# Optimization experiments

Measured on AMD Instinct MI355X. Metric: run time of the kernel, lower is better.

The kernel has to match this reference:

```python
import jax, jax.numpy as jnp
import numpy as np

B, S, D, H = 4, 2048, 512, 8
HD = D // H  # head_size = 64


def setup_inputs() -> dict:
    key = jax.random.key(0)
    ks = jax.random.split(key, 11)
    sd = 1.0 / np.sqrt(D)
    return {
        "q": jax.random.normal(ks[0], (B, S, D), jnp.float32),
        "k": jax.random.normal(ks[1], (B, S, D), jnp.float32),
        "v": jax.random.normal(ks[2], (B, S, D), jnp.float32),
        "Wq": jax.random.normal(ks[3], (D, D), jnp.float32) * sd,
        "bq": jnp.zeros((D,), jnp.float32),
        "Wk": jax.random.normal(ks[4], (D, D), jnp.float32) * sd,
        "bk": jnp.zeros((D,), jnp.float32),
        "Wv": jax.random.normal(ks[5], (D, D), jnp.float32) * sd,
        "bv": jnp.zeros((D,), jnp.float32),
        "Wo": jax.random.normal(ks[6], (D, D), jnp.float32) * sd,
        "bo": jnp.zeros((D,), jnp.float32),
    }


def _split_heads(x):
    # [B,S,D] -> [B,H,S,HD]
    return x.reshape(B, S, H, HD).transpose(0, 2, 1, 3)


def reference(q, k, v, Wq, bq, Wk, bk, Wv, bv, Wo, bo):
    qp = _split_heads(q @ Wq.T + bq)
    kp = _split_heads(k @ Wk.T + bk)
    vp = _split_heads(v @ Wv.T + bv)
    scale = 1.0 / jnp.sqrt(jnp.float32(HD))
    scores = jnp.einsum("bhqd,bhkd->bhqk", qp, kp) * scale  # [B,H,S,S]
    weights = jax.nn.softmax(scores, axis=-1)
    ctx = jnp.einsum("bhqk,bhkd->bhqd", weights, vp)
    ctx = ctx.transpose(0, 2, 1, 3).reshape(B, S, D)
    return ctx @ Wo.T + bo
```

## Files before the change

kernel.cpp:

```cpp
#include <hip/hip_runtime.h>
#include <hip/hip_bf16.h>
#include <stdint.h>

#define BB   4
#define SS   2048
#define DDIM 512
#define HH   8
#define HDIM 64
#define MTOT (BB*SS)
#define QSCALE (0.125f * 1.44269504088896340736f)

typedef __bf16 bf16;
typedef __bf16 bf16x8 __attribute__((ext_vector_type(8)));
typedef float  f32x4  __attribute__((ext_vector_type(4)));

__device__ __forceinline__ f32x4 mfma32(bf16x8 a, bf16x8 b, f32x4 c) {
    return __builtin_amdgcn_mfma_f32_16x16x32_bf16(a, b, c, 0, 0, 0);
}

__device__ __forceinline__ void gload_lds16(const void* g, void* l) {
    __builtin_amdgcn_global_load_lds(
        (__attribute__((address_space(1))) unsigned int*)(uintptr_t)g,
        (__attribute__((address_space(3))) unsigned int*)l,
        16, 0, 0);
}

__device__ __forceinline__ short bf16bits(float f) {
    union { __bf16 h; short s; } u; u.h = (__bf16)f; return u.s;
}

__global__ void cvt_kernel(const float* __restrict__ q, const float* __restrict__ k,
                           const float* __restrict__ v, const float* __restrict__ w0,
                           const float* __restrict__ w1, const float* __restrict__ w2,
                           const float* __restrict__ w3,
                           bf16* __restrict__ dq, bf16* __restrict__ dk,
                           bf16* __restrict__ dv, bf16* __restrict__ dw0,
                           bf16* __restrict__ dw1, bf16* __restrict__ dw2,
                           bf16* __restrict__ dw3) {
    const float* s; bf16* d; int n4;
    switch (blockIdx.y) {
        case 0: s = q;  d = dq;  n4 = (BB*SS*DDIM)/4; break;
        case 1: s = k;  d = dk;  n4 = (BB*SS*DDIM)/4; break;
        case 2: s = v;  d = dv;  n4 = (BB*SS*DDIM)/4; break;
        case 3: s = w0; d = dw0; n4 = (DDIM*DDIM)/4; break;
        case 4: s = w1; d = dw1; n4 = (DDIM*DDIM)/4; break;
        case 5: s = w2; d = dw2; n4 = (DDIM*DDIM)/4; break;
        default: s = w3; d = dw3; n4 = (DDIM*DDIM)/4; break;
    }
    int stride = gridDim.x * blockDim.x;
    for (int i = blockIdx.x * blockDim.x + threadIdx.x; i < n4; i += stride) {
        float4 f = ((const float4*)s)[i];
        union { bf16 h[4]; uint2 u; } o;
        o.h[0] = (bf16)f.x; o.h[1] = (bf16)f.y; o.h[2] = (bf16)f.z; o.h[3] = (bf16)f.w;
        ((uint2*)d)[i] = o.u;
    }
}

#define GEMM_BODY(A_, W_, K_, MB_, NB_)                                          \
    __shared__ bf16 As[2][128 * 64];                                             \
    __shared__ bf16 Bs[2][128 * 64];                                             \
    const int tid = threadIdx.x;                                                 \
    const int w = tid >> 6, lane = tid & 63;                                     \
    const int c15 = lane & 15, quad = lane >> 4;                                 \
    const int mblk = (MB_), nblk = (NB_);                                        \
    const int wm = (w & 1) * 64, wn = (w >> 1) * 64;                             \
    f32x4 acc[4][4] = {};                                                        \
    const bf16* Ablk = (A_) + (size_t)mblk * (K_);                               \
    const bf16* Bblk = (W_) + (size_t)nblk * (K_);                               \
    int g_off[4], l_base[4];                                                     \
    _Pragma("unroll")                                                            \
    for (int ci = 0; ci < 4; ++ci) {                                             \
        const int s = (w * 4 + ci) * 64 + lane;                                  \
        const int kr = s >> 3, kc = (s & 7) ^ (kr & 7);                          \
        g_off[ci] = kr * (K_) + kc * 8;                                          \
        l_base[ci] = (w * 4 + ci) * 512;                                         \
    }                                                                            \
    _Pragma("unroll")                                                            \
    for (int ci = 0; ci < 4; ++ci) {                                             \
        gload_lds16(Ablk + g_off[ci], &As[0][l_base[ci]]);                       \
        gload_lds16(Bblk + g_off[ci], &Bs[0][l_base[ci]]);                       \
    }                                                                            \
    int bufi = 0;                                                                \
    for (int kt = 0; kt < (K_); kt += 64) {                                      \
        __syncthreads();              \
        if (kt + 64 < (K_)) {                                                    \
            _Pragma("unroll")                                                    \
            for (int ci = 0; ci < 4; ++ci) {                                     \
                gload_lds16(Ablk + g_off[ci] + kt + 64, &As[bufi ^ 1][l_base[ci]]); \
                gload_lds16(Bblk + g_off[ci] + kt + 64, &Bs[bufi ^ 1][l_base[ci]]); \
            }                                                                    \
        }                                                                        \
        _Pragma("unroll")                                                        \
        for (int hh = 0; hh < 2; ++hh) {                                         \
            bf16x8 af[4], bfr[4];                                                \
            _Pragma("unroll")                                                    \
            for (int i = 0; i < 4; ++i) {                                        \
                const int row = wm + i * 16 + c15;                               \
                af[i] = *(const bf16x8*)&As[bufi][row * 64 + (((hh * 4 + quad) ^ (row & 7)) * 8)]; \
            }                                                                    \
            _Pragma("unroll")                                                    \
            for (int j = 0; j < 4; ++j) {                                        \
                const int row = wn + j * 16 + c15;                               \
                bfr[j] = *(const bf16x8*)&Bs[bufi][row * 64 + (((hh * 4 + quad) ^ (row & 7)) * 8)]; \
            }                                                                    \
            _Pragma("unroll")                                                    \
            for (int i = 0; i < 4; ++i)                                          \
                _Pragma("unroll")                                                \
                for (int j = 0; j < 4; ++j)                                      \
                    acc[i][j] = mfma32(af[i], bfr[j], acc[i][j]);                \
        }                                                                        \
        bufi ^= 1;                                                               \
    }

__global__ __launch_bounds__(256)
void proj_gemm(const bf16* __restrict__ Aq, const bf16* __restrict__ Ak,
               const bf16* __restrict__ Av,
               const bf16* __restrict__ Wq, const bf16* __restrict__ Wk,
               const bf16* __restrict__ Wv,
               const float* __restrict__ bq, const float* __restrict__ bk,
               const float* __restrict__ bv,
               bf16* __restrict__ Qp, bf16* __restrict__ Kp, bf16* __restrict__ Vt2) {
    const int mode = blockIdx.z;
    const bf16* A;  const bf16* Wm; const float* bias;
    int mb, nb;
    if (mode == 0)      { A = Aq; Wm = Wq; bias = bq; mb = blockIdx.x * 128; nb = blockIdx.y * 128; }
    else if (mode == 1) { A = Ak; Wm = Wk; bias = bk; mb = blockIdx.x * 128; nb = blockIdx.y * 128; }
    else {
        const int id = blockIdx.y * 64 + blockIdx.x;
        A = Wv; Wm = Av; bias = bv; mb = (id & 3) * 128; nb = (id >> 2) * 128;
    }
    GEMM_BODY(A, Wm, DDIM, mb, nb)
    if (mode == 2) {
        #pragma unroll
        for (int i = 0; i < 4; ++i) {
            #pragma unroll
            for (int r = 0; r < 4; ++r) {
                const int row = mblk + wm + i * 16 + quad * 4 + r;
                const float bval = bias[row];
                #pragma unroll
                for (int j = 0; j < 4; ++j) {
                    const int col = nblk + wn + j * 16 + c15;
                    const int colp = (col & ~31) + (c15 >> 2) * 8 + (j & 1) * 4 + (c15 & 3);
                    Vt2[(size_t)row * MTOT + colp] = (bf16)(acc[i][j][r] + bval);
                }
            }
        }
    } else {
        #pragma unroll
        for (int j = 0; j < 4; ++j) {
            const int col = nblk + wn + j * 16 + c15;
            const int h = col >> 6, hd = col & 63;
            const float bval = bias[col];
            #pragma unroll
            for (int i = 0; i < 4; ++i) {
                #pragma unroll
                for (int r = 0; r < 4; ++r) {
                    const int row = mblk + wm + i * 16 + quad * 4 + r;
                    const int b = row >> 11, s = row & (SS - 1);
                    float v = acc[i][j][r] + bval;
                    if (mode == 0) v *= QSCALE;
                    bf16* dst = (mode == 0) ? Qp : Kp;
                    dst[(((size_t)(b * HH + h)) * SS + s) * HDIM + hd] = (bf16)v;
                }
            }
        }
    }
}

__global__ __launch_bounds__(256)
void out_gemm(const bf16* __restrict__ A, const bf16* __restrict__ Wo,
              const float* __restrict__ bo, float* __restrict__ Out) {
    GEMM_BODY(A, Wo, DDIM, blockIdx.x * 128, blockIdx.y * 128)
    #pragma unroll
    for (int j = 0; j < 4; ++j) {
        const int col = nblk + wn + j * 16 + c15;
        const float bval = bo[col];
        #pragma unroll
        for (int i = 0; i < 4; ++i) {
            #pragma unroll
            for (int r = 0; r < 4; ++r) {
                const int row = mblk + wm + i * 16 + quad * 4 + r;
                Out[(size_t)row * DDIM + col] = acc[i][j][r] + bval;
            }
        }
    }
}

__global__ __launch_bounds__(256, 2)
void attn_kernel(const bf16* __restrict__ Qp, const bf16* __restrict__ Kp,
                 const bf16* __restrict__ Vt2, bf16* __restrict__ Ctx) {
    __shared__ bf16 Klds[2][128 * 64];
    __shared__ bf16 Vlds[2][64 * 128];

    const int tid = threadIdx.x;
    const int w = tid >> 6, lane = tid & 63;
    const int c15 = lane & 15, quad = lane >> 4;
    const int bh = blockIdx.y;
    const int b = bh >> 3, h = bh & 7;
    const int qbase = blockIdx.x * 128;

    const bf16* Qh = Qp + (size_t)bh * SS * HDIM;
    const bf16* Kh = Kp + (size_t)bh * SS * HDIM;
    const bf16* Vh = Vt2 + (size_t)h * HDIM * MTOT + (size_t)b * SS;

    bf16x8 qf[2][2];
    #pragma unroll
    for (int g = 0; g < 2; ++g) {
        const int qrow = qbase + w * 32 + g * 16 + c15;
        qf[g][0] = *(const bf16x8*)&Qh[(size_t)qrow * HDIM + quad * 8];
        qf[g][1] = *(const bf16x8*)&Qh[(size_t)qrow * HDIM + 32 + quad * 8];
    }

    int koff[4], voff[4];
    #pragma unroll
    for (int ci = 0; ci < 4; ++ci) {
        const int s = (w * 4 + ci) * 64 + lane;
        const int kr = s >> 3, kc = (s & 7) ^ (kr & 7);
        koff[ci] = kr * HDIM + kc * 8;
        const int vr = s >> 4, vc = (s & 15) ^ (vr & 15);
        voff[ci] = vr * MTOT + vc * 8;
    }

    union FragS { short s[8]; bf16x8 v; };
    FragS idf, ones8;
    #pragma unroll
    for (int j = 0; j < 8; ++j) {
        idf.s[j] = (j < 4 && quad * 4 + j == c15) ? (short)0x3F80 : (short)0;
        ones8.s[j] = (short)0x3F80;
    }

    f32x4 oacc[2][4] = {};
    f32x4 lacc[2] = {};
    const int ksw = c15 & 7;

    #pragma unroll
    for (int ci = 0; ci < 4; ++ci) {
        gload_lds16(Kh + koff[ci], &Klds[0][(w * 4 + ci) * 512]);
        gload_lds16(Vh + voff[ci], &Vlds[0][(w * 4 + ci) * 512]);
    }

    int buf = 0;
    for (int kt = 0; kt < SS; kt += 128) {
        __syncthreads();
        if (kt + 128 < SS) {
            const bf16* Ks = Kh + (size_t)(kt + 128) * HDIM;
            const bf16* Vs = Vh + (kt + 128);
            #pragma unroll
            for (int ci = 0; ci < 4; ++ci) {
                gload_lds16(Ks + koff[ci], &Klds[buf ^ 1][(w * 4 + ci) * 512]);
                gload_lds16(Vs + voff[ci], &Vlds[buf ^ 1][(w * 4 + ci) * 512]);
            }
        }

        FragS paf[2][4];
        #pragma unroll
        for (int nt = 0; nt < 8; ++nt) {
            const int krow = nt * 16 + c15;
            bf16x8 kb0 = *(const bf16x8*)&Klds[buf][(krow * 8 + (quad ^ ksw)) * 8];
            bf16x8 kb1 = *(const bf16x8*)&Klds[buf][(krow * 8 + ((quad + 4) ^ ksw)) * 8];
            #pragma unroll
            for (int g = 0; g < 2; ++g) {
                f32x4 z = {};
                z = mfma32(qf[g][0], kb0, z);
                z = mfma32(qf[g][1], kb1, z);
                FragS pk;
                #pragma unroll
                for (int r = 0; r < 4; ++r)
                    pk.s[r] = bf16bits(__builtin_amdgcn_exp2f(z[r]));
                pk.s[4] = pk.s[5] = pk.s[6] = pk.s[7] = 0;
                f32x4 zero = {};
                f32x4 t = mfma32(pk.v, idf.v, zero);
                const int half = (nt & 1) * 4;
                #pragma unroll
                for (int r = 0; r < 4; ++r)
                    paf[g][nt >> 1].s[half + r] = bf16bits(t[r]);
            }
        }

        #pragma unroll
        for (int t = 0; t < 4; ++t) {
            lacc[0] = mfma32(paf[0][t].v, ones8.v, lacc[0]);
            lacc[1] = mfma32(paf[1][t].v, ones8.v, lacc[1]);
            #pragma unroll
            for (int j = 0; j < 4; ++j) {
                const int row = j * 16 + c15;
                bf16x8 vb = *(const bf16x8*)&Vlds[buf][row * 128 +
                            (((4 * t + quad) ^ c15) * 8)];
                oacc[0][j] = mfma32(paf[0][t].v, vb, oacc[0][j]);
                oacc[1][j] = mfma32(paf[1][t].v, vb, oacc[1][j]);
            }
        }
        buf ^= 1;
    }

    bf16* Cb = Ctx + ((size_t)b * SS) * DDIM + (size_t)h * HDIM;
    #pragma unroll
    for (int g = 0; g < 2; ++g)
        #pragma unroll
        for (int r = 0; r < 4; ++r) {
            const int row = qbase + w * 32 + g * 16 + quad * 4 + r;
            const float inv = 1.0f / lacc[g][r];
            #pragma unroll
            for (int j = 0; j < 4; ++j) {
                const int hd = j * 16 + c15;
                Cb[(size_t)row * DDIM + hd] = (bf16)(oacc[g][j][r] * inv);
            }
        }
}

extern "C" void kernel_launch(void* const* d_in, const int* in_sizes, int n_in,
                              void* d_out, int out_size, void* d_ws, size_t ws_size,
                              hipStream_t stream) {
    const float* q  = (const float*)d_in[0];
    const float* k  = (const float*)d_in[1];
    const float* v  = (const float*)d_in[2];
    const float* Wq = (const float*)d_in[3];
    const float* bq = (const float*)d_in[4];
    const float* Wk = (const float*)d_in[5];
    const float* bk = (const float*)d_in[6];
    const float* Wv = (const float*)d_in[7];
    const float* bv = (const float*)d_in[8];
    const float* Wo = (const float*)d_in[9];
    const float* bo = (const float*)d_in[10];
    float* out = (float*)d_out;

    const size_t SZ_T = (size_t)BB * SS * DDIM * 2;
    const size_t SZ_W = (size_t)DDIM * DDIM * 2;
    char* ws = (char*)d_ws;
    bf16* qb  = (bf16*)(ws + 0 * SZ_T);
    bf16* kb  = (bf16*)(ws + 1 * SZ_T);
    bf16* vb  = (bf16*)(ws + 2 * SZ_T);
    bf16* Wqb = (bf16*)(ws + 3 * SZ_T + 0 * SZ_W);
    bf16* Wkb = (bf16*)(ws + 3 * SZ_T + 1 * SZ_W);
    bf16* Wvb = (bf16*)(ws + 3 * SZ_T + 2 * SZ_W);
    bf16* Wob = (bf16*)(ws + 3 * SZ_T + 3 * SZ_W);
    bf16* Qp  = (bf16*)(ws + 3 * SZ_T + 4 * SZ_W);
    bf16* Kp  = (bf16*)(ws + 4 * SZ_T + 4 * SZ_W);
    bf16* Vt2 = (bf16*)(ws + 5 * SZ_T + 4 * SZ_W);
    bf16* ctx = (bf16*)(ws + 6 * SZ_T + 4 * SZ_W);
    const size_t needed = 7 * SZ_T + 4 * SZ_W;
    if (ws_size < needed) return;

    cvt_kernel<<<dim3(512, 7), 256, 0, stream>>>(q, k, v, Wq, Wk, Wv, Wo,
                                                 qb, kb, vb, Wqb, Wkb, Wvb, Wob);
    proj_gemm<<<dim3(MTOT / 128, DDIM / 128, 3), 256, 0, stream>>>(
        qb, kb, vb, Wqb, Wkb, Wvb, bq, bk, bv, Qp, Kp, Vt2);
    attn_kernel<<<dim3(SS / 128, BB * HH), 256, 0, stream>>>(Qp, Kp, Vt2, ctx);
    out_gemm<<<dim3(MTOT / 128, DDIM / 128), 256, 0, stream>>>(ctx, Wob, bo, out);
}
```

Before: 191.6 us.

## Fuse fp32-to-bf16 conversion into GEMM loads and drop identity-MFMA transpose in attention

Removes the separate conversion kernel. The projection and output GEMMs now load fp32 inputs into registers, convert them to bf16, and write them to LDS inside the double-buffered loop. In attention, the QK MFMA operands are swapped so the score fragment comes out already in the layout the PV MFMA needs, which removes the exp/identity-MFMA transpose step. This cuts a full bf16 round trip of q, k and v through HBM and some MFMA work, at the cost of register-staged loads instead of direct-to-LDS loads in the projection GEMM.

```diff
diff --git a/kernel.cpp b/kernel.cpp
--- a/kernel.cpp
+++ b/kernel.cpp
@@ -29,34 +29,14 @@
     union { __bf16 h; short s; } u; u.h = (__bf16)f; return u.s;
 }
 
-__global__ void cvt_kernel(const float* __restrict__ q, const float* __restrict__ k,
-                           const float* __restrict__ v, const float* __restrict__ w0,
-                           const float* __restrict__ w1, const float* __restrict__ w2,
-                           const float* __restrict__ w3,
-                           bf16* __restrict__ dq, bf16* __restrict__ dk,
-                           bf16* __restrict__ dv, bf16* __restrict__ dw0,
-                           bf16* __restrict__ dw1, bf16* __restrict__ dw2,
-                           bf16* __restrict__ dw3) {
-    const float* s; bf16* d; int n4;
-    switch (blockIdx.y) {
-        case 0: s = q;  d = dq;  n4 = (BB*SS*DDIM)/4; break;
-        case 1: s = k;  d = dk;  n4 = (BB*SS*DDIM)/4; break;
-        case 2: s = v;  d = dv;  n4 = (BB*SS*DDIM)/4; break;
-        case 3: s = w0; d = dw0; n4 = (DDIM*DDIM)/4; break;
-        case 4: s = w1; d = dw1; n4 = (DDIM*DDIM)/4; break;
-        case 5: s = w2; d = dw2; n4 = (DDIM*DDIM)/4; break;
-        default: s = w3; d = dw3; n4 = (DDIM*DDIM)/4; break;
-    }
-    int stride = gridDim.x * blockDim.x;
-    for (int i = blockIdx.x * blockDim.x + threadIdx.x; i < n4; i += stride) {
-        float4 f = ((const float4*)s)[i];
-        union { bf16 h[4]; uint2 u; } o;
-        o.h[0] = (bf16)f.x; o.h[1] = (bf16)f.y; o.h[2] = (bf16)f.z; o.h[3] = (bf16)f.w;
-        ((uint2*)d)[i] = o.u;
-    }
-}
-
-#define GEMM_BODY(A_, W_, K_, MB_, NB_)                                          \
+__device__ __forceinline__ void cvt_write8(float4 a, float4 b, bf16* dst) {
+    union { bf16 h[8]; uint4 u; } o;
+    o.h[0] = (bf16)a.x; o.h[1] = (bf16)a.y; o.h[2] = (bf16)a.z; o.h[3] = (bf16)a.w;
+    o.h[4] = (bf16)b.x; o.h[5] = (bf16)b.y; o.h[6] = (bf16)b.z; o.h[7] = (bf16)b.w;
+    *(uint4*)dst = o.u;
+}
+
+#define GEMM_CORE(A_, AF32_, W_, WF32_, K_, MB_, NB_)                            \
     __shared__ bf16 As[2][128 * 64];                                             \
     __shared__ bf16 Bs[2][128 * 64];                                             \
     const int tid = threadIdx.x;                                                 \
@@ -65,29 +45,50 @@
     const int mblk = (MB_), nblk = (NB_);                                        \
     const int wm = (w & 1) * 64, wn = (w >> 1) * 64;                             \
     f32x4 acc[4][4] = {};                                                        \
-    const bf16* Ablk = (A_) + (size_t)mblk * (K_);                               \
-    const bf16* Bblk = (W_) + (size_t)nblk * (K_);                               \
-    int g_off[4], l_base[4];                                                     \
+    int soff[4], goff[4];                                                        \
     _Pragma("unroll")                                                            \
     for (int ci = 0; ci < 4; ++ci) {                                             \
         const int s = (w * 4 + ci) * 64 + lane;                                  \
         const int kr = s >> 3, kc = (s & 7) ^ (kr & 7);                          \
-        g_off[ci] = kr * (K_) + kc * 8;                                          \
-        l_base[ci] = (w * 4 + ci) * 512;                                         \
+        soff[ci] = s * 8;                                                        \
+        goff[ci] = kr * (K_) + kc * 8;                                           \
+    }                                                                            \
+    const float* ap32 = (const float*)(A_) + (size_t)mblk * (K_);                \
+    const float* bp32 = (const float*)(W_) + (size_t)nblk * (K_);                \
+    const bf16*  ap16 = (const bf16*)(A_) + (size_t)mblk * (K_);                 \
+    const bf16*  bp16 = (const bf16*)(W_) + (size_t)nblk * (K_);                 \
+    float4 areg[4][2], breg[4][2];                                               \
+    _Pragma("unroll")                                                            \
+    for (int ci = 0; ci < 4; ++ci) {                                             \
+        if (AF32_) {                                                             \
+            areg[ci][0] = *(const float4*)(ap32 + goff[ci]);                     \
+            areg[ci][1] = *(const float4*)(ap32 + goff[ci] + 4);                 \
+        } else gload_lds16(ap16 + goff[ci], &As[0][soff[ci]]);                   \
+        if (WF32_) {                                                             \
+            breg[ci][0] = *(const float4*)(bp32 + goff[ci]);                     \
+            breg[ci][1] = *(const float4*)(bp32 + goff[ci] + 4);                 \
+        } else gload_lds16(bp16 + goff[ci], &Bs[0][soff[ci]]);                   \
     }                                                                            \
     _Pragma("unroll")                                                            \
     for (int ci = 0; ci < 4; ++ci) {                                             \
-        gload_lds16(Ablk + g_off[ci], &As[0][l_base[ci]]);                       \
-        gload_lds16(Bblk + g_off[ci], &Bs[0][l_base[ci]]);                       \
+        if (AF32_) cvt_write8(areg[ci][0], areg[ci][1], &As[0][soff[ci]]);       \
+        if (WF32_) cvt_write8(breg[ci][0], breg[ci][1], &Bs[0][soff[ci]]);       \
     }                                                                            \
     int bufi = 0;                                                                \
     for (int kt = 0; kt < (K_); kt += 64) {                                      \
-        __syncthreads();              \
-        if (kt + 64 < (K_)) {                                                    \
+        __syncthreads();                                                         \
+        const bool more = (kt + 64 < (K_));                                      \
+        if (more) {                                                              \
             _Pragma("unroll")                                                    \
             for (int ci = 0; ci < 4; ++ci) {                                     \
-                gload_lds16(Ablk + g_off[ci] + kt + 64, &As[bufi ^ 1][l_base[ci]]); \
-                gload_lds16(Bblk + g_off[ci] + kt + 64, &Bs[bufi ^ 1][l_base[ci]]); \
+                if (AF32_) {                                                     \
+                    areg[ci][0] = *(const float4*)(ap32 + goff[ci] + kt + 64);   \
+                    areg[ci][1] = *(const float4*)(ap32 + goff[ci] + kt + 68);   \
+                } else gload_lds16(ap16 + goff[ci] + kt + 64, &As[bufi ^ 1][soff[ci]]); \
+                if (WF32_) {                                                     \
+                    breg[ci][0] = *(const float4*)(bp32 + goff[ci] + kt + 64);   \
+                    breg[ci][1] = *(const float4*)(bp32 + goff[ci] + kt + 68);   \
+                } else gload_lds16(bp16 + goff[ci] + kt + 64, &Bs[bufi ^ 1][soff[ci]]); \
             }                                                                    \
         }                                                                        \
         _Pragma("unroll")                                                        \
@@ -109,27 +110,34 @@
                 for (int j = 0; j < 4; ++j)                                      \
                     acc[i][j] = mfma32(af[i], bfr[j], acc[i][j]);                \
         }                                                                        \
+        if (more) {                                                              \
+            _Pragma("unroll")                                                    \
+            for (int ci = 0; ci < 4; ++ci) {                                     \
+                if (AF32_) cvt_write8(areg[ci][0], areg[ci][1], &As[bufi ^ 1][soff[ci]]); \
+                if (WF32_) cvt_write8(breg[ci][0], breg[ci][1], &Bs[bufi ^ 1][soff[ci]]); \
+            }                                                                    \
+        }                                                                        \
         bufi ^= 1;                                                               \
     }
 
 __global__ __launch_bounds__(256)
-void proj_gemm(const bf16* __restrict__ Aq, const bf16* __restrict__ Ak,
-               const bf16* __restrict__ Av,
-               const bf16* __restrict__ Wq, const bf16* __restrict__ Wk,
-               const bf16* __restrict__ Wv,
+void proj_gemm(const float* __restrict__ q, const float* __restrict__ k,
+               const float* __restrict__ v,
+               const float* __restrict__ Wq, const float* __restrict__ Wk,
+               const float* __restrict__ Wv,
                const float* __restrict__ bq, const float* __restrict__ bk,
                const float* __restrict__ bv,
                bf16* __restrict__ Qp, bf16* __restrict__ Kp, bf16* __restrict__ Vt2) {
     const int mode = blockIdx.z;
-    const bf16* A;  const bf16* Wm; const float* bias;
+    const float* A; const float* Wm; const float* bias;
     int mb, nb;
-    if (mode == 0)      { A = Aq; Wm = Wq; bias = bq; mb = blockIdx.x * 128; nb = blockIdx.y * 128; }
-    else if (mode == 1) { A = Ak; Wm = Wk; bias = bk; mb = blockIdx.x * 128; nb = blockIdx.y * 128; }
+    if (mode == 0)      { A = q; Wm = Wq; bias = bq; mb = blockIdx.x * 128; nb = blockIdx.y * 128; }
+    else if (mode == 1) { A = k; Wm = Wk; bias = bk; mb = blockIdx.x * 128; nb = blockIdx.y * 128; }
     else {
         const int id = blockIdx.y * 64 + blockIdx.x;
-        A = Wv; Wm = Av; bias = bv; mb = (id & 3) * 128; nb = (id >> 2) * 128;
-    }
-    GEMM_BODY(A, Wm, DDIM, mb, nb)
+        A = Wv; Wm = v; bias = bv; mb = (id & 3) * 128; nb = (id >> 2) * 128;
+    }
+    GEMM_CORE(A, 1, Wm, 1, DDIM, mb, nb)
     if (mode == 2) {
         #pragma unroll
         for (int i = 0; i < 4; ++i) {
@@ -157,10 +165,10 @@
                 for (int r = 0; r < 4; ++r) {
                     const int row = mblk + wm + i * 16 + quad * 4 + r;
                     const int b = row >> 11, s = row & (SS - 1);
-                    float v = acc[i][j][r] + bval;
-                    if (mode == 0) v *= QSCALE;
+                    float vv = acc[i][j][r] + bval;
+                    if (mode == 0) vv *= QSCALE;
                     bf16* dst = (mode == 0) ? Qp : Kp;
-                    dst[(((size_t)(b * HH + h)) * SS + s) * HDIM + hd] = (bf16)v;
+                    dst[(((size_t)(b * HH + h)) * SS + s) * HDIM + hd] = (bf16)vv;
                 }
             }
         }
@@ -168,9 +176,9 @@
 }
 
 __global__ __launch_bounds__(256)
-void out_gemm(const bf16* __restrict__ A, const bf16* __restrict__ Wo,
+void out_gemm(const bf16* __restrict__ A, const float* __restrict__ Wo,
               const float* __restrict__ bo, float* __restrict__ Out) {
-    GEMM_BODY(A, Wo, DDIM, blockIdx.x * 128, blockIdx.y * 128)
+    GEMM_CORE(A, 0, Wo, 1, DDIM, blockIdx.x * 128, blockIdx.y * 128)
     #pragma unroll
     for (int j = 0; j < 4; ++j) {
         const int col = nblk + wn + j * 16 + c15;
@@ -222,12 +230,9 @@
     }
 
     union FragS { short s[8]; bf16x8 v; };
-    FragS idf, ones8;
-    #pragma unroll
-    for (int j = 0; j < 8; ++j) {
-        idf.s[j] = (j < 4 && quad * 4 + j == c15) ? (short)0x3F80 : (short)0;
-        ones8.s[j] = (short)0x3F80;
-    }
+    FragS ones8;
+    #pragma unroll
+    for (int j = 0; j < 8; ++j) ones8.s[j] = (short)0x3F80;
 
     f32x4 oacc[2][4] = {};
     f32x4 lacc[2] = {};
@@ -261,19 +266,13 @@
             #pragma unroll
             for (int g = 0; g < 2; ++g) {
                 f32x4 z = {};
-                z = mfma32(qf[g][0], kb0, z);
-                z = mfma32(qf[g][1], kb1, z);
-                FragS pk;
-                #pragma unroll
-                for (int r = 0; r < 4; ++r)
-                    pk.s[r] = bf16bits(__builtin_amdgcn_exp2f(z[r]));
-                pk.s[4] = pk.s[5] = pk.s[6] = pk.s[7] = 0;
-                f32x4 zero = {};
-                f32x4 t = mfma32(pk.v, idf.v, zero);
+                z = mfma32(kb0, qf[g][0], z);
+                z = mfma32(kb1, qf[g][1], z);
                 const int half = (nt & 1) * 4;
                 #pragma unroll
                 for (int r = 0; r < 4; ++r)
-                    paf[g][nt >> 1].s[half + r] = bf16bits(t[r]);
+                    paf[g][nt >> 1].s[half + r] =
+                        bf16bits(__builtin_amdgcn_exp2f(z[r]));
             }
         }
 
@@ -325,26 +324,16 @@
     float* out = (float*)d_out;
 
     const size_t SZ_T = (size_t)BB * SS * DDIM * 2;
-    const size_t SZ_W = (size_t)DDIM * DDIM * 2;
     char* ws = (char*)d_ws;
-    bf16* qb  = (bf16*)(ws + 0 * SZ_T);
-    bf16* kb  = (bf16*)(ws + 1 * SZ_T);
-    bf16* vb  = (bf16*)(ws + 2 * SZ_T);
-    bf16* Wqb = (bf16*)(ws + 3 * SZ_T + 0 * SZ_W);
-    bf16* Wkb = (bf16*)(ws + 3 * SZ_T + 1 * SZ_W);
-    bf16* Wvb = (bf16*)(ws + 3 * SZ_T + 2 * SZ_W);
-    bf16* Wob = (bf16*)(ws + 3 * SZ_T + 3 * SZ_W);
-    bf16* Qp  = (bf16*)(ws + 3 * SZ_T + 4 * SZ_W);
-    bf16* Kp  = (bf16*)(ws + 4 * SZ_T + 4 * SZ_W);
-    bf16* Vt2 = (bf16*)(ws + 5 * SZ_T + 4 * SZ_W);
-    bf16* ctx = (bf16*)(ws + 6 * SZ_T + 4 * SZ_W);
-    const size_t needed = 7 * SZ_T + 4 * SZ_W;
+    bf16* Qp  = (bf16*)(ws + 0 * SZ_T);
+    bf16* Kp  = (bf16*)(ws + 1 * SZ_T);
+    bf16* Vt2 = (bf16*)(ws + 2 * SZ_T);
+    bf16* ctx = (bf16*)(ws + 3 * SZ_T);
+    const size_t needed = 4 * SZ_T;
     if (ws_size < needed) return;
 
-    cvt_kernel<<<dim3(512, 7), 256, 0, stream>>>(q, k, v, Wq, Wk, Wv, Wo,
-                                                 qb, kb, vb, Wqb, Wkb, Wvb, Wob);
     proj_gemm<<<dim3(MTOT / 128, DDIM / 128, 3), 256, 0, stream>>>(
-        qb, kb, vb, Wqb, Wkb, Wvb, bq, bk, bv, Qp, Kp, Vt2);
+        q, k, v, Wq, Wk, Wv, bq, bk, bv, Qp, Kp, Vt2);
     attn_kernel<<<dim3(SS / 128, BB * HH), 256, 0, stream>>>(Qp, Kp, Vt2, ctx);
-    out_gemm<<<dim3(MTOT / 128, DDIM / 128), 256, 0, stream>>>(ctx, Wob, bo, out);
-}
+    out_gemm<<<dim3(MTOT / 128, DDIM / 128), 256, 0, stream>>>(ctx, Wo, bo, out);
+}
```

Result: no change. 190.3 us (-0.7%).

## Swap QK MFMA operands to drop identity transpose; halve GEMM K-tile

Applied to the files above, without the earlier changes.

In the attention loop, the QK^T MFMA now takes K as the A operand and Q as the B operand. The exp2 results therefore land directly in the layout the PV MFMA needs as its A fragment. This removes the per-tile identity-matrix MFMA and its extra bf16 conversions, which existed only to transpose the probabilities. Separately, the projection and output GEMMs shrink their K tile from 64 to 32 with a matching LDS swizzle and set launch bounds for 4 blocks per SU. That cuts LDS per block so more blocks can be resident, at the cost of twice as many barriers per GEMM.

```diff
diff --git a/kernel.cpp b/kernel.cpp
--- a/kernel.cpp
+++ b/kernel.cpp
@@ -56,80 +56,78 @@
     }
 }
 
-#define GEMM_BODY(A_, W_, K_, MB_, NB_)                                          \
-    __shared__ bf16 As[2][128 * 64];                                             \
-    __shared__ bf16 Bs[2][128 * 64];                                             \
+#define GEMM_CORE(A_, W_, K_, MB_, NB_)                                          \
+    __shared__ bf16 As[2][128 * 32];                                             \
+    __shared__ bf16 Bs[2][128 * 32];                                             \
     const int tid = threadIdx.x;                                                 \
     const int w = tid >> 6, lane = tid & 63;                                     \
     const int c15 = lane & 15, quad = lane >> 4;                                 \
     const int mblk = (MB_), nblk = (NB_);                                        \
     const int wm = (w & 1) * 64, wn = (w >> 1) * 64;                             \
     f32x4 acc[4][4] = {};                                                        \
-    const bf16* Ablk = (A_) + (size_t)mblk * (K_);                               \
-    const bf16* Bblk = (W_) + (size_t)nblk * (K_);                               \
-    int g_off[4], l_base[4];                                                     \
+    const bf16* Ab = (A_) + (size_t)mblk * (K_);                                 \
+    const bf16* Bb = (W_) + (size_t)nblk * (K_);                                 \
+    int goff[2], soff[2];                                                        \
     _Pragma("unroll")                                                            \
-    for (int ci = 0; ci < 4; ++ci) {                                             \
-        const int s = (w * 4 + ci) * 64 + lane;                                  \
-        const int kr = s >> 3, kc = (s & 7) ^ (kr & 7);                          \
-        g_off[ci] = kr * (K_) + kc * 8;                                          \
-        l_base[ci] = (w * 4 + ci) * 512;                                         \
+    for (int ci = 0; ci < 2; ++ci) {                                             \
+        const int s = (w * 2 + ci) * 64 + lane;                 \
+        const int kr = s >> 2;                                                   \
+        const int c = (s & 3) ^ ((kr >> 1) & 3);                                 \
+        goff[ci] = kr * (K_) + c * 8;                                            \
+        soff[ci] = s * 8;                                                        \
     }                                                                            \
     _Pragma("unroll")                                                            \
-    for (int ci = 0; ci < 4; ++ci) {                                             \
-        gload_lds16(Ablk + g_off[ci], &As[0][l_base[ci]]);                       \
-        gload_lds16(Bblk + g_off[ci], &Bs[0][l_base[ci]]);                       \
+    for (int ci = 0; ci < 2; ++ci) {                                             \
+        gload_lds16(Ab + goff[ci], &As[0][soff[ci]]);                            \
+        gload_lds16(Bb + goff[ci], &Bs[0][soff[ci]]);                            \
     }                                                                            \
     int bufi = 0;                                                                \
-    for (int kt = 0; kt < (K_); kt += 64) {                                      \
+    for (int kt = 0; kt < (K_); kt += 32) {                                      \
         __syncthreads();              \
-        if (kt + 64 < (K_)) {                                                    \
+        if (kt + 32 < (K_)) {                                                    \
             _Pragma("unroll")                                                    \
-            for (int ci = 0; ci < 4; ++ci) {                                     \
-                gload_lds16(Ablk + g_off[ci] + kt + 64, &As[bufi ^ 1][l_base[ci]]); \
-                gload_lds16(Bblk + g_off[ci] + kt + 64, &Bs[bufi ^ 1][l_base[ci]]); \
+            for (int ci = 0; ci < 2; ++ci) {                                     \
+                gload_lds16(Ab + goff[ci] + kt + 32, &As[bufi ^ 1][soff[ci]]);   \
+                gload_lds16(Bb + goff[ci] + kt + 32, &Bs[bufi ^ 1][soff[ci]]);   \
             }                                                                    \
         }                                                                        \
+        bf16x8 af[4], bfr[4];                                                    \
         _Pragma("unroll")                                                        \
-        for (int hh = 0; hh < 2; ++hh) {                                         \
-            bf16x8 af[4], bfr[4];                                                \
+        for (int i = 0; i < 4; ++i) {                                            \
+            const int row = wm + i * 16 + c15;                                   \
+            af[i] = *(const bf16x8*)&As[bufi][row * 32 + ((quad ^ ((row >> 1) & 3)) * 8)]; \
+        }                                                                        \
+        _Pragma("unroll")                                                        \
+        for (int j = 0; j < 4; ++j) {                                            \
+            const int row = wn + j * 16 + c15;                                   \
+            bfr[j] = *(const bf16x8*)&Bs[bufi][row * 32 + ((quad ^ ((row >> 1) & 3)) * 8)]; \
+        }                                                                        \
+        _Pragma("unroll")                                                        \
+        for (int i = 0; i < 4; ++i)                                              \
             _Pragma("unroll")                                                    \
-            for (int i = 0; i < 4; ++i) {                                        \
-                const int row = wm + i * 16 + c15;                               \
-                af[i] = *(const bf16x8*)&As[bufi][row * 64 + (((hh * 4 + quad) ^ (row & 7)) * 8)]; \
-            }                                                                    \
-            _Pragma("unroll")                                                    \
-            for (int j = 0; j < 4; ++j) {                                        \
-                const int row = wn + j * 16 + c15;                               \
-                bfr[j] = *(const bf16x8*)&Bs[bufi][row * 64 + (((hh * 4 + quad) ^ (row & 7)) * 8)]; \
-            }                                                                    \
-            _Pragma("unroll")                                                    \
-            for (int i = 0; i < 4; ++i)                                          \
-                _Pragma("unroll")                                                \
-                for (int j = 0; j < 4; ++j)                                      \
-                    acc[i][j] = mfma32(af[i], bfr[j], acc[i][j]);                \
-        }                                                                        \
+            for (int j = 0; j < 4; ++j)                                          \
+                acc[i][j] = mfma32(af[i], bfr[j], acc[i][j]);                    \
         bufi ^= 1;                                                               \
     }
 
-__global__ __launch_bounds__(256)
-void proj_gemm(const bf16* __restrict__ Aq, const bf16* __restrict__ Ak,
-               const bf16* __restrict__ Av,
+__global__ __launch_bounds__(256, 4)
+void proj_gemm(const bf16* __restrict__ qb, const bf16* __restrict__ kb,
+               const bf16* __restrict__ vb,
                const bf16* __restrict__ Wq, const bf16* __restrict__ Wk,
                const bf16* __restrict__ Wv,
                const float* __restrict__ bq, const float* __restrict__ bk,
                const float* __restrict__ bv,
                bf16* __restrict__ Qp, bf16* __restrict__ Kp, bf16* __restrict__ Vt2) {
     const int mode = blockIdx.z;
-    const bf16* A;  const bf16* Wm; const float* bias;
+    const bf16* A; const bf16* Wm; const float* bias;
     int mb, nb;
-    if (mode == 0)      { A = Aq; Wm = Wq; bias = bq; mb = blockIdx.x * 128; nb = blockIdx.y * 128; }
-    else if (mode == 1) { A = Ak; Wm = Wk; bias = bk; mb = blockIdx.x * 128; nb = blockIdx.y * 128; }
+    if (mode == 0)      { A = qb; Wm = Wq; bias = bq; mb = blockIdx.x * 128; nb = blockIdx.y * 128; }
+    else if (mode == 1) { A = kb; Wm = Wk; bias = bk; mb = blockIdx.x * 128; nb = blockIdx.y * 128; }
     else {
         const int id = blockIdx.y * 64 + blockIdx.x;
-        A = Wv; Wm = Av; bias = bv; mb = (id & 3) * 128; nb = (id >> 2) * 128;
-    }
-    GEMM_BODY(A, Wm, DDIM, mb, nb)
+        A = Wv; Wm = vb; bias = bv; mb = (id & 3) * 128; nb = (id >> 2) * 128;
+    }
+    GEMM_CORE(A, Wm, DDIM, mb, nb)
     if (mode == 2) {
         #pragma unroll
         for (int i = 0; i < 4; ++i) {
@@ -157,20 +155,20 @@
                 for (int r = 0; r < 4; ++r) {
                     const int row = mblk + wm + i * 16 + quad * 4 + r;
                     const int b = row >> 11, s = row & (SS - 1);
-                    float v = acc[i][j][r] + bval;
-                    if (mode == 0) v *= QSCALE;
+                    float vv = acc[i][j][r] + bval;
+                    if (mode == 0) vv *= QSCALE;
                     bf16* dst = (mode == 0) ? Qp : Kp;
-                    dst[(((size_t)(b * HH + h)) * SS + s) * HDIM + hd] = (bf16)v;
+                    dst[(((size_t)(b * HH + h)) * SS + s) * HDIM + hd] = (bf16)vv;
                 }
             }
         }
     }
 }
 
-__global__ __launch_bounds__(256)
+__global__ __launch_bounds__(256, 4)
 void out_gemm(const bf16* __restrict__ A, const bf16* __restrict__ Wo,
               const float* __restrict__ bo, float* __restrict__ Out) {
-    GEMM_BODY(A, Wo, DDIM, blockIdx.x * 128, blockIdx.y * 128)
+    GEMM_CORE(A, Wo, DDIM, blockIdx.x * 128, blockIdx.y * 128)
     #pragma unroll
     for (int j = 0; j < 4; ++j) {
         const int col = nblk + wn + j * 16 + c15;
@@ -222,12 +220,9 @@
     }
 
     union FragS { short s[8]; bf16x8 v; };
-    FragS idf, ones8;
-    #pragma unroll
-    for (int j = 0; j < 8; ++j) {
-        idf.s[j] = (j < 4 && quad * 4 + j == c15) ? (short)0x3F80 : (short)0;
-        ones8.s[j] = (short)0x3F80;
-    }
+    FragS ones8;
+    #pragma unroll
+    for (int j = 0; j < 8; ++j) ones8.s[j] = (short)0x3F80;
 
     f32x4 oacc[2][4] = {};
     f32x4 lacc[2] = {};
@@ -261,19 +256,13 @@
             #pragma unroll
             for (int g = 0; g < 2; ++g) {
                 f32x4 z = {};
-                z = mfma32(qf[g][0], kb0, z);
-                z = mfma32(qf[g][1], kb1, z);
-                FragS pk;
-                #pragma unroll
-                for (int r = 0; r < 4; ++r)
-                    pk.s[r] = bf16bits(__builtin_amdgcn_exp2f(z[r]));
-                pk.s[4] = pk.s[5] = pk.s[6] = pk.s[7] = 0;
-                f32x4 zero = {};
-                f32x4 t = mfma32(pk.v, idf.v, zero);
+                z = mfma32(kb0, qf[g][0], z);
+                z = mfma32(kb1, qf[g][1], z);
                 const int half = (nt & 1) * 4;
                 #pragma unroll
                 for (int r = 0; r < 4; ++r)
-                    paf[g][nt >> 1].s[half + r] = bf16bits(t[r]);
+                    paf[g][nt >> 1].s[half + r] =
+                        bf16bits(__builtin_amdgcn_exp2f(z[r]));
             }
         }
 
@@ -284,10 +273,10 @@
             #pragma unroll
             for (int j = 0; j < 4; ++j) {
                 const int row = j * 16 + c15;
-                bf16x8 vb = *(const bf16x8*)&Vlds[buf][row * 128 +
-                            (((4 * t + quad) ^ c15) * 8)];
-                oacc[0][j] = mfma32(paf[0][t].v, vb, oacc[0][j]);
-                oacc[1][j] = mfma32(paf[1][t].v, vb, oacc[1][j]);
+                bf16x8 vbf = *(const bf16x8*)&Vlds[buf][row * 128 +
+                             (((4 * t + quad) ^ c15) * 8)];
+                oacc[0][j] = mfma32(paf[0][t].v, vbf, oacc[0][j]);
+                oacc[1][j] = mfma32(paf[1][t].v, vbf, oacc[1][j]);
             }
         }
         buf ^= 1;
```

After: 182.7 us. 1.05x faster.
